# Optimization experiments

Hardware: AMD Instinct MI355X
Metric: run time of the kernel (lower is better)

## Reference

```python
import jax, jax.numpy as jnp
import numpy as np

N_NODES = 50000
N_EDGES = 800000
G_DIM = 128
H1_DIM = 128
H2_DIM = 128
N_REL = 8          # 2 * n_speakers**2, n_speakers = 2
N_BASES = 30


def setup_inputs() -> dict:
    key = jax.random.key(0)
    ks = jax.random.split(key, 10)
    node_features = jax.random.normal(ks[0], (N_NODES, G_DIM), jnp.float32)
    edge_index = jax.random.randint(ks[1], (2, N_EDGES), 0, N_NODES, jnp.int32)
    edge_norm = jax.random.uniform(ks[2], (N_EDGES,), jnp.float32)
    edge_type = jax.random.randint(ks[3], (N_EDGES,), 0, N_REL, jnp.int32)
    # RGCN basis-decomposition params
    w_comp = jax.random.normal(ks[4], (N_REL, N_BASES), jnp.float32) / np.sqrt(N_BASES)
    bases = jax.random.normal(ks[5], (N_BASES, G_DIM, H1_DIM), jnp.float32) / np.sqrt(G_DIM)
    loop_weight = jax.random.normal(ks[6], (G_DIM, H1_DIM), jnp.float32) / np.sqrt(G_DIM)
    bias1 = jnp.zeros((H1_DIM,), jnp.float32)
    # GraphConv params
    W2 = jax.random.normal(ks[7], (H1_DIM, H2_DIM), jnp.float32) / np.sqrt(H1_DIM)
    bias2 = jnp.zeros((H2_DIM,), jnp.float32)
    return dict(node_features=node_features, edge_index=edge_index,
                edge_norm=edge_norm, edge_type=edge_type,
                w_comp=w_comp, bases=bases, loop_weight=loop_weight, bias1=bias1,
                W2=W2, bias2=bias2)


def reference(node_features, edge_index, edge_norm, edge_type,
              w_comp, bases, loop_weight, bias1, W2, bias2):
    N = node_features.shape[0]
    src, dst = edge_index[0], edge_index[1]

    # ---- RGCNConv (DGL RelGraphConv, basis regularizer, self_loop + bias) ----
    # relation weights from bases: [R, g, h1]
    weight = jnp.einsum('rb,bio->rio', w_comp, bases)
    # project all nodes by every relation (R is small), then gather per edge
    xw = jnp.einsum('ni,rio->rno', node_features, weight)   # [R, N, h1]
    msgs = xw[edge_type, src] * edge_norm[:, None]          # [E, h1]
    agg = jax.ops.segment_sum(msgs, dst, num_segments=N)    # scatter-add to dst
    h = agg + node_features @ loop_weight + bias1           # [N, h1]

    # ---- GraphConv (DGL, norm='both', edge_weight; degrees are UNweighted) ----
    ones = jnp.ones_like(edge_norm)
    out_deg = jax.ops.segment_sum(ones, src, num_segments=N)
    in_deg = jax.ops.segment_sum(ones, dst, num_segments=N)
    norm_src = jnp.clip(out_deg, 1.0) ** -0.5               # [N]
    norm_dst = jnp.clip(in_deg, 1.0) ** -0.5                # [N]
    m2 = (h * norm_src[:, None])[src] * edge_norm[:, None]  # [E, h1]
    agg2 = jax.ops.segment_sum(m2, dst, num_segments=N)     # [N, h1]
    out = (agg2 * norm_dst[:, None]) @ W2 + bias2           # [N, h2]
    return out
```

## Files before the change

### kernel.cpp

```cpp
#include <hip/hip_runtime.h>

#define NN 50000
#define EE 800000
#define NB 30
#define NJ 1152
#define NSB 49
#define NPART 16
#define RANGE 3136
#define NSLICE 64
#define ESL 12500
#define NPAD 50176

typedef __attribute__((ext_vector_type(8))) short short8;
typedef __attribute__((ext_vector_type(4))) float f32x4;

__device__ __forceinline__ unsigned short f2bf(float f) {
  unsigned u = __float_as_uint(f);
  u += 0x7FFF + ((u >> 16) & 1);
  return (unsigned short)(u >> 16);
}
__device__ __forceinline__ float bf2f(unsigned short s) {
  return __uint_as_float(((unsigned)s) << 16);
}

__global__ __launch_bounds__(256) void k_prep(const float* __restrict__ wcomp,
                                              const float* __restrict__ bases,
                                              const float* __restrict__ loopw,
                                              const float* __restrict__ W2,
                                              const float* __restrict__ X,
                                              unsigned short* __restrict__ Wt,
                                              unsigned short* __restrict__ W2t,
                                              unsigned short* __restrict__ Xbf) {
  int b = blockIdx.x;
  if (b < 576) {
    int idx = b * 256 + threadIdx.x;
    int j = idx >> 7, k = idx & 127;
    float v;
    if (j < 1024) {
      int r = j >> 7, o = j & 127;
      float s = 0.f;
#pragma unroll
      for (int bb = 0; bb < NB; ++bb)
        s = fmaf(wcomp[r * NB + bb], bases[((size_t)bb * 128 + k) * 128 + o], s);
      v = s;
    } else {
      v = loopw[k * 128 + (j - 1024)];
    }
    Wt[idx] = f2bf(v);
    if (idx < 128 * 128) W2t[idx] = f2bf(W2[k * 128 + j]);
  } else {
    int i = ((b - 576) * 256 + threadIdx.x) * 4;
    float4 v = *(const float4*)(X + i);
    uint2 o;
    o.x = (unsigned)f2bf(v.x) | ((unsigned)f2bf(v.y) << 16);
    o.y = (unsigned)f2bf(v.z) | ((unsigned)f2bf(v.w) << 16);
    *(uint2*)(Xbf + i) = o;
  }
}

__global__ __launch_bounds__(256) void k_hist(const int* __restrict__ EI,
                                              int* __restrict__ pdin, int* __restrict__ pdout) {
  __shared__ int hist[RANGE];
  int b = blockIdx.x;
  int kind = b & 1;
  int sl = (b >> 1) & (NSLICE - 1);
  int r = b >> 7;
  const int base = r * RANGE;
  const int* vals = kind ? EI : EI + EE;
  int* part = kind ? pdout : pdin;
  for (int j = threadIdx.x; j < RANGE; j += 256) hist[j] = 0;
  __syncthreads();
  const int e0 = sl * ESL;
  for (int i = threadIdx.x; i < ESL / 4; i += 256) {
    int4 d = *(const int4*)(vals + e0 + i * 4);
    int x;
    x = d.x - base; if ((unsigned)x < RANGE) atomicAdd(&hist[x], 1);
    x = d.y - base; if ((unsigned)x < RANGE) atomicAdd(&hist[x], 1);
    x = d.z - base; if ((unsigned)x < RANGE) atomicAdd(&hist[x], 1);
    x = d.w - base; if ((unsigned)x < RANGE) atomicAdd(&hist[x], 1);
  }
  __syncthreads();
  for (int j = threadIdx.x; j < RANGE; j += 256)
    part[sl * NPAD + base + j] = hist[j];
}

__global__ __launch_bounds__(256) void k_scan_a(const int* __restrict__ pdin,
                                                const int* __restrict__ pdout,
                                                int* __restrict__ din,
                                                int* __restrict__ dout,
                                                int* __restrict__ bsum) {
  __shared__ int wsum[4];
  int b = blockIdx.x, t = threadIdx.x;
  int lane = t & 63, w = t >> 6;
  int i0 = b * 1024 + t * 4;
  int4 acc = {0, 0, 0, 0}, od = {0, 0, 0, 0};
  for (int sl = 0; sl < NSLICE; ++sl) {
    int4 a = *(const int4*)(pdin + sl * NPAD + i0);
    int4 o = *(const int4*)(pdout + sl * NPAD + i0);
    acc.x += a.x; acc.y += a.y; acc.z += a.z; acc.w += a.w;
    od.x += o.x; od.y += o.y; od.z += o.z; od.w += o.w;
  }
  *(int4*)(din + i0) = acc;
  *(int4*)(dout + i0) = od;
  int sv = acc.x + acc.y + acc.z + acc.w;
#pragma unroll
  for (int off = 32; off; off >>= 1) sv += __shfl_down(sv, off, 64);
  if (lane == 0) wsum[w] = sv;
  __syncthreads();
  if (t == 0) bsum[b] = wsum[0] + wsum[1] + wsum[2] + wsum[3];
}

__global__ void k_scan_b(int* __restrict__ bsum, int* __restrict__ row_ptr) {
  int t = threadIdx.x;
  int v = (t < NSB) ? bsum[t] : 0;
  int orig = v;
#pragma unroll
  for (int off = 1; off < 64; off <<= 1) {
    int u = __shfl_up(v, off, 64);
    if (t >= off) v += u;
  }
  if (t < NSB) bsum[t] = v - orig;
  if (t == 0) row_ptr[NN] = EE;
}

__global__ __launch_bounds__(256) void k_scan_c(const int* __restrict__ din,
                                                const int* __restrict__ bsum,
                                                int* __restrict__ row_ptr) {
  __shared__ int wsum[4];
  int b = blockIdx.x, t = threadIdx.x;
  int lane = t & 63, w = t >> 6;
  int i0 = b * 1024 + t * 4;
  int4 d = *(const int4*)(din + i0);
  int sth = d.x + d.y + d.z + d.w;
  int v = sth;
#pragma unroll
  for (int off = 1; off < 64; off <<= 1) {
    int u = __shfl_up(v, off, 64);
    if (lane >= off) v += u;
  }
  if (lane == 63) wsum[w] = v;
  __syncthreads();
  int woff = 0;
  for (int j = 0; j < w; ++j) woff += wsum[j];
  int base = bsum[b] + woff + (v - sth);
  if (i0 + 0 <= NN) row_ptr[i0 + 0] = base; base += d.x;
  if (i0 + 1 <= NN) row_ptr[i0 + 1] = base; base += d.y;
  if (i0 + 2 <= NN) row_ptr[i0 + 2] = base; base += d.z;
  if (i0 + 3 <= NN) row_ptr[i0 + 3] = base;
}

__global__ __launch_bounds__(256) void k_pfx(int* __restrict__ pdin,
                                             const int* __restrict__ row_ptr) {
  int n = blockIdx.x * 256 + threadIdx.x;
  int run = row_ptr[n];
#pragma unroll 8
  for (int sl = 0; sl < NSLICE; ++sl) {
    int c = pdin[sl * NPAD + n];
    pdin[sl * NPAD + n] = run;
    run += c;
  }
}

__global__ __launch_bounds__(256) void k_scatter(const int* __restrict__ src,
                                                 const int* __restrict__ dst,
                                                 const int* __restrict__ ety,
                                                 const float* __restrict__ enorm,
                                                 const int* __restrict__ pdin,
                                                 int2* __restrict__ em1) {
  __shared__ int cur[RANGE];
  int b = blockIdx.x;
  int sl = b & (NSLICE - 1), r = b >> 6;
  const int base = r * RANGE;
  for (int j = threadIdx.x; j < RANGE; j += 256)
    cur[j] = pdin[sl * NPAD + base + j];
  __syncthreads();
  const int e0 = sl * ESL;
  for (int i = threadIdx.x; i < ESL / 4; i += 256) {
    int4 d = *(const int4*)(dst + e0 + i * 4);
    int vals[4] = {d.x, d.y, d.z, d.w};
#pragma unroll
    for (int j = 0; j < 4; ++j) {
      int dv = vals[j] - base;
      if ((unsigned)dv < RANGE) {
        int e = e0 + i * 4 + j;
        int pos = atomicAdd(&cur[dv], 1);
        int sv = src[e];
        int wb = __float_as_int(enorm[e]);
        em1[pos] = make_int2(sv * NJ + ety[e] * 128, wb);
      }
    }
  }
}

__global__ __launch_bounds__(256) void k_gemm(const unsigned short* __restrict__ A,
                                              const unsigned short* __restrict__ B,
                                              unsigned short* __restrict__ Cbf,
                                              float* __restrict__ Cf,
                                              const float* __restrict__ bias,
                                              int M, int ldc) {
  __shared__ unsigned short As[128 * 136];
  __shared__ unsigned short Bs[128 * 136];
  const int m0 = blockIdx.x * 128, j0 = blockIdx.y * 128;
  const int t = threadIdx.x;
  for (int i = t; i < 2048; i += 256) {
    int r = i >> 4, c = i & 15;
    uint4 va = {0, 0, 0, 0};
    int gr = m0 + r;
    if (gr < M) va = *(const uint4*)(A + (size_t)gr * 128 + c * 8);
    *(uint4*)(&As[r * 136 + c * 8]) = va;
    uint4 vb = *(const uint4*)(B + (size_t)(j0 + r) * 128 + c * 8);
    *(uint4*)(&Bs[r * 136 + c * 8]) = vb;
  }
  __syncthreads();

  const int lane = t & 63, wave = t >> 6;
  const int wr = (wave >> 1) * 64, wc = (wave & 1) * 64;
  const int lr = lane & 15, lk = (lane >> 4) * 8;

  f32x4 acc[4][4];
#pragma unroll
  for (int m = 0; m < 4; ++m)
#pragma unroll
    for (int n = 0; n < 4; ++n) acc[m][n] = (f32x4){0.f, 0.f, 0.f, 0.f};

#pragma unroll
  for (int kt = 0; kt < 4; ++kt) {
    short8 af[4], bfr[4];
#pragma unroll
    for (int m = 0; m < 4; ++m)
      af[m] = *(const short8*)(&As[(wr + m * 16 + lr) * 136 + kt * 32 + lk]);
#pragma unroll
    for (int n = 0; n < 4; ++n)
      bfr[n] = *(const short8*)(&Bs[(wc + n * 16 + lr) * 136 + kt * 32 + lk]);
#pragma unroll
    for (int m = 0; m < 4; ++m)
#pragma unroll
      for (int n = 0; n < 4; ++n)
        acc[m][n] = __builtin_amdgcn_mfma_f32_16x16x32_bf16(af[m], bfr[n], acc[m][n], 0, 0, 0);
  }

#pragma unroll
  for (int m = 0; m < 4; ++m) {
    int rbase = m0 + wr + m * 16 + (lane >> 4) * 4;
#pragma unroll
    for (int i = 0; i < 4; ++i) {
      int row = rbase + i;
      if (row >= M) continue;
      if (Cbf) {
        unsigned short* cr = Cbf + (size_t)row * ldc + j0 + wc;
#pragma unroll
        for (int n = 0; n < 4; ++n) cr[n * 16 + lr] = f2bf(acc[m][n][i]);
      } else {
        float* cr = Cf + (size_t)row * ldc + j0 + wc;
#pragma unroll
        for (int n = 0; n < 4; ++n) cr[n * 16 + lr] = acc[m][n][i] + bias[j0 + wc + n * 16 + lr];
      }
    }
  }
}

#define UNR 8

__global__ __launch_bounds__(256) void k_agg1(const unsigned short* __restrict__ xw,
                                              const int2* __restrict__ em1,
                                              const int* __restrict__ row_ptr,
                                              const int* __restrict__ deg_out,
                                              const float* __restrict__ bias1,
                                              unsigned short* __restrict__ hs) {
  int gw = (blockIdx.x * blockDim.x + threadIdx.x) >> 6;
  int lane = threadIdx.x & 63;
  if (gw >= NN) return;
  int beg = row_ptr[gw], end = row_ptr[gw + 1];
  float a0 = 0.f, a1 = 0.f;
  for (int i = beg; i < end; i += UNR) {
    int2 md[UNR];
    unsigned v[UNR];
#pragma unroll
    for (int j = 0; j < UNR; ++j) {
      int idx = i + j;
      idx = idx < end ? idx : end - 1;
      md[j] = em1[idx];
      if (i + j >= end) md[j].y = 0;
    }
#pragma unroll
    for (int j = 0; j < UNR; ++j)
      v[j] = *(const unsigned*)(xw + (size_t)(unsigned)md[j].x + lane * 2);
#pragma unroll
    for (int j = 0; j < UNR; ++j) {
      float w = __int_as_float(md[j].y);
      a0 = fmaf(w, bf2f((unsigned short)(v[j] & 0xffff)), a0);
      a1 = fmaf(w, bf2f((unsigned short)(v[j] >> 16)), a1);
    }
  }
  unsigned vl = *(const unsigned*)(xw + (size_t)gw * NJ + 1024 + lane * 2);
  float ns = rsqrtf(fmaxf((float)deg_out[gw], 1.f));
  float h0 = (a0 + bf2f((unsigned short)(vl & 0xffff)) + bias1[lane * 2]) * ns;
  float h1 = (a1 + bf2f((unsigned short)(vl >> 16)) + bias1[lane * 2 + 1]) * ns;
  unsigned o = (unsigned)f2bf(h0) | ((unsigned)f2bf(h1) << 16);
  *(unsigned*)(hs + (size_t)gw * 128 + lane * 2) = o;
}

__global__ __launch_bounds__(256) void k_agg2(const unsigned short* __restrict__ hs,
                                              const int2* __restrict__ em1,
                                              const int* __restrict__ row_ptr,
                                              unsigned short* __restrict__ zb) {
  int gw = (blockIdx.x * blockDim.x + threadIdx.x) >> 6;
  int lane = threadIdx.x & 63;
  if (gw >= NN) return;
  int beg = row_ptr[gw], end = row_ptr[gw + 1];
  float a0 = 0.f, a1 = 0.f;
  for (int i = beg; i < end; i += UNR) {
    int2 md[UNR];
    unsigned v[UNR];
#pragma unroll
    for (int j = 0; j < UNR; ++j) {
      int idx = i + j;
      idx = idx < end ? idx : end - 1;
      md[j] = em1[idx];
      if (i + j >= end) md[j].y = 0;
    }
#pragma unroll
    for (int j = 0; j < UNR; ++j) {
      unsigned srcn = (((unsigned)md[j].x) >> 7) / 9u;
      v[j] = *(const unsigned*)(hs + ((size_t)srcn << 7) + lane * 2);
    }
#pragma unroll
    for (int j = 0; j < UNR; ++j) {
      float w = __int_as_float(md[j].y);
      a0 = fmaf(w, bf2f((unsigned short)(v[j] & 0xffff)), a0);
      a1 = fmaf(w, bf2f((unsigned short)(v[j] >> 16)), a1);
    }
  }
  float nd = rsqrtf(fmaxf((float)(end - beg), 1.f));
  unsigned o = (unsigned)f2bf(a0 * nd) | ((unsigned)f2bf(a1 * nd) << 16);
  *(unsigned*)(zb + (size_t)gw * 128 + lane * 2) = o;
}

extern "C" void kernel_launch(void* const* d_in, const int* in_sizes, int n_in,
                              void* d_out, int out_size, void* d_ws, size_t ws_size,
                              hipStream_t stream) {
  const float* X = (const float*)d_in[0];
  const int* EI = (const int*)d_in[1];
  const float* enorm = (const float*)d_in[2];
  const int* etype = (const int*)d_in[3];
  const float* wcomp = (const float*)d_in[4];
  const float* bases = (const float*)d_in[5];
  const float* loopw = (const float*)d_in[6];
  const float* bias1 = (const float*)d_in[7];
  const float* W2 = (const float*)d_in[8];
  const float* bias2 = (const float*)d_in[9];
  float* out = (float*)d_out;
  const int* srcA = EI;
  const int* dstA = EI + EE;

  char* p = (char*)d_ws;
  auto alloc = [&](size_t bytes) {
    char* r = p;
    p += (bytes + 255) & ~(size_t)255;
    return r;
  };
  unsigned short* xw  = (unsigned short*)alloc((size_t)NN * NJ * 2);
  unsigned short* Xbf = (unsigned short*)alloc((size_t)NN * 128 * 2);
  unsigned short* hs  = (unsigned short*)alloc((size_t)NN * 128 * 2);
  unsigned short* zb  = (unsigned short*)alloc((size_t)NN * 128 * 2);
  unsigned short* Wt  = (unsigned short*)alloc((size_t)NJ * 128 * 2);
  unsigned short* W2t = (unsigned short*)alloc(128 * 128 * 2);
  int* pdin    = (int*)alloc((size_t)NSLICE * NPAD * 4);
  int* pdout   = (int*)alloc((size_t)NSLICE * NPAD * 4);
  int* din     = (int*)alloc((size_t)NPAD * 4);
  int* dout    = (int*)alloc((size_t)NPAD * 4);
  int* row_ptr = (int*)alloc((size_t)(NPAD + 1) * 4);
  int* bsum    = (int*)alloc((size_t)NSB * 4);
  int2* em1    = (int2*)alloc((size_t)EE * 8);

  hipLaunchKernelGGL(k_prep, dim3(6826), dim3(256), 0, stream,
                     wcomp, bases, loopw, W2, X, Wt, W2t, Xbf);
  hipLaunchKernelGGL(k_hist, dim3(2048), dim3(256), 0, stream, EI, pdin, pdout);
  hipLaunchKernelGGL(k_scan_a, dim3(NSB), dim3(256), 0, stream, pdin, pdout, din, dout, bsum);
  hipLaunchKernelGGL(k_scan_b, dim3(1), dim3(64), 0, stream, bsum, row_ptr);
  hipLaunchKernelGGL(k_scan_c, dim3(NSB), dim3(256), 0, stream, din, bsum, row_ptr);
  hipLaunchKernelGGL(k_pfx, dim3(NPAD / 256), dim3(256), 0, stream, pdin, row_ptr);
  hipLaunchKernelGGL(k_scatter, dim3(1024), dim3(256), 0, stream,
                     srcA, dstA, etype, enorm, pdin, em1);
  hipLaunchKernelGGL(k_gemm, dim3(391, 9), dim3(256), 0, stream,
                     Xbf, Wt, xw, (float*)nullptr, (const float*)nullptr, NN, NJ);
  hipLaunchKernelGGL(k_agg1, dim3(12500), dim3(256), 0, stream,
                     xw, em1, row_ptr, dout, bias1, hs);
  hipLaunchKernelGGL(k_agg2, dim3(12500), dim3(256), 0, stream,
                     hs, em1, row_ptr, zb);
  hipLaunchKernelGGL(k_gemm, dim3(391, 1), dim3(256), 0, stream,
                     zb, W2t, (unsigned short*)nullptr, out, bias2, NN, 128);
}
```

Before: 325.3 us.

## Aggregate raw features per relation first, then apply stacked relation weights via GEMM

Reorders layer-1 RGCN as aggregate-then-transform. Each destination node gathers bf16 input features (256 B rows) and accumulates per-relation sums into a [N,8*128] buffer. A single K=1152 GEMM then applies the stacked relation and self-loop weights, fusing bias and source-degree normalization into its epilogue. This replaces the gather of 128-wide rows from the large 50000x1152 projected table, which has a poor cache footprint, with gathers from a much smaller table. The cost is more FMAs per edge (8 masked relation accumulators), a 100 MB intermediate write and read, and an extra K loop in the GEMM.

```diff
diff --git a/kernel.cpp b/kernel.cpp
--- a/kernel.cpp
+++ b/kernel.cpp
@@ -3,7 +3,7 @@
 #define NN 50000
 #define EE 800000
 #define NB 30
-#define NJ 1152
+#define NK2 1152
 #define NSB 49
 #define NPART 16
 #define RANGE 3136
@@ -28,26 +28,30 @@
                                               const float* __restrict__ loopw,
                                               const float* __restrict__ W2,
                                               const float* __restrict__ X,
-                                              unsigned short* __restrict__ Wt,
+                                              unsigned short* __restrict__ Wt2,
                                               unsigned short* __restrict__ W2t,
                                               unsigned short* __restrict__ Xbf) {
   int b = blockIdx.x;
   if (b < 576) {
     int idx = b * 256 + threadIdx.x;
-    int j = idx >> 7, k = idx & 127;
+    int o = idx & 127;
+    int ri = idx >> 7;
+    int r = ri >> 7, i = ri & 127;
     float v;
-    if (j < 1024) {
-      int r = j >> 7, o = j & 127;
+    if (r < 8) {
       float s = 0.f;
 #pragma unroll
       for (int bb = 0; bb < NB; ++bb)
-        s = fmaf(wcomp[r * NB + bb], bases[((size_t)bb * 128 + k) * 128 + o], s);
+        s = fmaf(wcomp[r * NB + bb], bases[((size_t)bb * 128 + i) * 128 + o], s);
       v = s;
     } else {
-      v = loopw[k * 128 + (j - 1024)];
-    }
-    Wt[idx] = f2bf(v);
-    if (idx < 128 * 128) W2t[idx] = f2bf(W2[k * 128 + j]);
+      v = loopw[i * 128 + o];
+    }
+    Wt2[(size_t)o * NK2 + ri] = f2bf(v);
+    if (idx < 128 * 128) {
+      int j = idx >> 7, k = idx & 127;
+      W2t[idx] = f2bf(W2[k * 128 + j]);
+    }
   } else {
     int i = ((b - 576) * 256 + threadIdx.x) * 4;
     float4 v = *(const float4*)(X + i);
@@ -166,7 +170,7 @@
                                                  const int* __restrict__ ety,
                                                  const float* __restrict__ enorm,
                                                  const int* __restrict__ pdin,
-                                                 int2* __restrict__ em1) {
+                                                 int2* __restrict__ em) {
   __shared__ int cur[RANGE];
   int b = blockIdx.x;
   int sl = b & (NSLICE - 1), r = b >> 6;
@@ -184,94 +188,25 @@
       if ((unsigned)dv < RANGE) {
         int e = e0 + i * 4 + j;
         int pos = atomicAdd(&cur[dv], 1);
-        int sv = src[e];
-        int wb = __float_as_int(enorm[e]);
-        em1[pos] = make_int2(sv * NJ + ety[e] * 128, wb);
+        em[pos] = make_int2((src[e] << 4) | ety[e], __float_as_int(enorm[e]));
       }
     }
   }
 }
 
-__global__ __launch_bounds__(256) void k_gemm(const unsigned short* __restrict__ A,
-                                              const unsigned short* __restrict__ B,
-                                              unsigned short* __restrict__ Cbf,
-                                              float* __restrict__ Cf,
-                                              const float* __restrict__ bias,
-                                              int M, int ldc) {
-  __shared__ unsigned short As[128 * 136];
-  __shared__ unsigned short Bs[128 * 136];
-  const int m0 = blockIdx.x * 128, j0 = blockIdx.y * 128;
-  const int t = threadIdx.x;
-  for (int i = t; i < 2048; i += 256) {
-    int r = i >> 4, c = i & 15;
-    uint4 va = {0, 0, 0, 0};
-    int gr = m0 + r;
-    if (gr < M) va = *(const uint4*)(A + (size_t)gr * 128 + c * 8);
-    *(uint4*)(&As[r * 136 + c * 8]) = va;
-    uint4 vb = *(const uint4*)(B + (size_t)(j0 + r) * 128 + c * 8);
-    *(uint4*)(&Bs[r * 136 + c * 8]) = vb;
-  }
-  __syncthreads();
-
-  const int lane = t & 63, wave = t >> 6;
-  const int wr = (wave >> 1) * 64, wc = (wave & 1) * 64;
-  const int lr = lane & 15, lk = (lane >> 4) * 8;
-
-  f32x4 acc[4][4];
-#pragma unroll
-  for (int m = 0; m < 4; ++m)
-#pragma unroll
-    for (int n = 0; n < 4; ++n) acc[m][n] = (f32x4){0.f, 0.f, 0.f, 0.f};
-
-#pragma unroll
-  for (int kt = 0; kt < 4; ++kt) {
-    short8 af[4], bfr[4];
-#pragma unroll
-    for (int m = 0; m < 4; ++m)
-      af[m] = *(const short8*)(&As[(wr + m * 16 + lr) * 136 + kt * 32 + lk]);
-#pragma unroll
-    for (int n = 0; n < 4; ++n)
-      bfr[n] = *(const short8*)(&Bs[(wc + n * 16 + lr) * 136 + kt * 32 + lk]);
-#pragma unroll
-    for (int m = 0; m < 4; ++m)
-#pragma unroll
-      for (int n = 0; n < 4; ++n)
-        acc[m][n] = __builtin_amdgcn_mfma_f32_16x16x32_bf16(af[m], bfr[n], acc[m][n], 0, 0, 0);
-  }
-
-#pragma unroll
-  for (int m = 0; m < 4; ++m) {
-    int rbase = m0 + wr + m * 16 + (lane >> 4) * 4;
-#pragma unroll
-    for (int i = 0; i < 4; ++i) {
-      int row = rbase + i;
-      if (row >= M) continue;
-      if (Cbf) {
-        unsigned short* cr = Cbf + (size_t)row * ldc + j0 + wc;
-#pragma unroll
-        for (int n = 0; n < 4; ++n) cr[n * 16 + lr] = f2bf(acc[m][n][i]);
-      } else {
-        float* cr = Cf + (size_t)row * ldc + j0 + wc;
-#pragma unroll
-        for (int n = 0; n < 4; ++n) cr[n * 16 + lr] = acc[m][n][i] + bias[j0 + wc + n * 16 + lr];
-      }
-    }
-  }
-}
-
 #define UNR 8
 
-__global__ __launch_bounds__(256) void k_agg1(const unsigned short* __restrict__ xw,
-                                              const int2* __restrict__ em1,
+__global__ __launch_bounds__(256) void k_agg0(const unsigned short* __restrict__ Xbf,
+                                              const int2* __restrict__ em,
                                               const int* __restrict__ row_ptr,
-                                              const int* __restrict__ deg_out,
-                                              const float* __restrict__ bias1,
-                                              unsigned short* __restrict__ hs) {
+                                              unsigned short* __restrict__ Y) {
   int gw = (blockIdx.x * blockDim.x + threadIdx.x) >> 6;
   int lane = threadIdx.x & 63;
   if (gw >= NN) return;
   int beg = row_ptr[gw], end = row_ptr[gw + 1];
-  float a0 = 0.f, a1 = 0.f;
+  float a0[8], a1[8];
+#pragma unroll
+  for (int r = 0; r < 8; ++r) { a0[r] = 0.f; a1[r] = 0.f; }
   for (int i = beg; i < end; i += UNR) {
     int2 md[UNR];
     unsigned v[UNR];
@@ -279,29 +214,107 @@
     for (int j = 0; j < UNR; ++j) {
       int idx = i + j;
       idx = idx < end ? idx : end - 1;
-      md[j] = em1[idx];
+      md[j] = em[idx];
       if (i + j >= end) md[j].y = 0;
     }
 #pragma unroll
     for (int j = 0; j < UNR; ++j)
-      v[j] = *(const unsigned*)(xw + (size_t)(unsigned)md[j].x + lane * 2);
+      v[j] = *(const unsigned*)(Xbf + ((size_t)((unsigned)md[j].x >> 4) << 7) + lane * 2);
 #pragma unroll
     for (int j = 0; j < UNR; ++j) {
       float w = __int_as_float(md[j].y);
-      a0 = fmaf(w, bf2f((unsigned short)(v[j] & 0xffff)), a0);
-      a1 = fmaf(w, bf2f((unsigned short)(v[j] >> 16)), a1);
-    }
-  }
-  unsigned vl = *(const unsigned*)(xw + (size_t)gw * NJ + 1024 + lane * 2);
-  float ns = rsqrtf(fmaxf((float)deg_out[gw], 1.f));
-  float h0 = (a0 + bf2f((unsigned short)(vl & 0xffff)) + bias1[lane * 2]) * ns;
-  float h1 = (a1 + bf2f((unsigned short)(vl >> 16)) + bias1[lane * 2 + 1]) * ns;
-  unsigned o = (unsigned)f2bf(h0) | ((unsigned)f2bf(h1) << 16);
-  *(unsigned*)(hs + (size_t)gw * 128 + lane * 2) = o;
+      int ty = md[j].x & 15;
+      float x0 = bf2f((unsigned short)(v[j] & 0xffff));
+      float x1 = bf2f((unsigned short)(v[j] >> 16));
+#pragma unroll
+      for (int r = 0; r < 8; ++r) {
+        float ws = (ty == r) ? w : 0.f;
+        a0[r] = fmaf(ws, x0, a0[r]);
+        a1[r] = fmaf(ws, x1, a1[r]);
+      }
+    }
+  }
+  unsigned short* yr = Y + (size_t)gw * 1024 + lane * 2;
+#pragma unroll
+  for (int r = 0; r < 8; ++r) {
+    unsigned o = (unsigned)f2bf(a0[r]) | ((unsigned)f2bf(a1[r]) << 16);
+    *(unsigned*)(yr + r * 128) = o;
+  }
+}
+
+__global__ __launch_bounds__(256) void k_gemmh(const unsigned short* __restrict__ Y,
+                                               const unsigned short* __restrict__ Xbf,
+                                               const unsigned short* __restrict__ Wt2,
+                                               const int* __restrict__ dout,
+                                               const float* __restrict__ bias1,
+                                               unsigned short* __restrict__ hs) {
+  __shared__ unsigned short As[64 * 136];
+  __shared__ unsigned short Bs[128 * 136];
+  const int m0 = blockIdx.x * 64;
+  const int t = threadIdx.x;
+  const int lane = t & 63, wave = t >> 6;
+  const int wr = (wave >> 1) * 32, wc = (wave & 1) * 64;
+  const int lr = lane & 15, lk = (lane >> 4) * 8;
+
+  f32x4 acc[2][4];
+#pragma unroll
+  for (int m = 0; m < 2; ++m)
+#pragma unroll
+    for (int n = 0; n < 4; ++n) acc[m][n] = (f32x4){0.f, 0.f, 0.f, 0.f};
+
+  for (int kt = 0; kt < 9; ++kt) {
+    __syncthreads();
+    for (int i = t; i < 1024; i += 256) {
+      int r = i >> 4, c = i & 15;
+      int n = m0 + r;
+      uint4 va = {0, 0, 0, 0};
+      if (n < NN) {
+        const unsigned short* ap = (kt < 8) ? (Y + (size_t)n * 1024 + kt * 128)
+                                            : (Xbf + (size_t)n * 128);
+        va = *(const uint4*)(ap + c * 8);
+      }
+      *(uint4*)(&As[r * 136 + c * 8]) = va;
+    }
+    for (int i = t; i < 2048; i += 256) {
+      int r = i >> 4, c = i & 15;
+      uint4 vb = *(const uint4*)(Wt2 + (size_t)r * NK2 + kt * 128 + c * 8);
+      *(uint4*)(&Bs[r * 136 + c * 8]) = vb;
+    }
+    __syncthreads();
+#pragma unroll
+    for (int s = 0; s < 4; ++s) {
+      short8 af[2], bfv[4];
+#pragma unroll
+      for (int m = 0; m < 2; ++m)
+        af[m] = *(const short8*)(&As[(wr + m * 16 + lr) * 136 + s * 32 + lk]);
+#pragma unroll
+      for (int n = 0; n < 4; ++n)
+        bfv[n] = *(const short8*)(&Bs[(wc + n * 16 + lr) * 136 + s * 32 + lk]);
+#pragma unroll
+      for (int m = 0; m < 2; ++m)
+#pragma unroll
+        for (int n = 0; n < 4; ++n)
+          acc[m][n] = __builtin_amdgcn_mfma_f32_16x16x32_bf16(af[m], bfv[n], acc[m][n], 0, 0, 0);
+    }
+  }
+
+#pragma unroll
+  for (int m = 0; m < 2; ++m) {
+#pragma unroll
+    for (int i = 0; i < 4; ++i) {
+      int row = m0 + wr + m * 16 + (lane >> 4) * 4 + i;
+      if (row >= NN) continue;
+      float ns = rsqrtf(fmaxf((float)dout[row], 1.f));
+      unsigned short* hr = hs + (size_t)row * 128 + wc;
+#pragma unroll
+      for (int n = 0; n < 4; ++n)
+        hr[n * 16 + lr] = f2bf((acc[m][n][i] + bias1[wc + n * 16 + lr]) * ns);
+    }
+  }
 }
 
 __global__ __launch_bounds__(256) void k_agg2(const unsigned short* __restrict__ hs,
-                                              const int2* __restrict__ em1,
+                                              const int2* __restrict__ em,
                                               const int* __restrict__ row_ptr,
                                               unsigned short* __restrict__ zb) {
   int gw = (blockIdx.x * blockDim.x + threadIdx.x) >> 6;
@@ -316,14 +329,12 @@
     for (int j = 0; j < UNR; ++j) {
       int idx = i + j;
       idx = idx < end ? idx : end - 1;
-      md[j] = em1[idx];
+      md[j] = em[idx];
       if (i + j >= end) md[j].y = 0;
     }
 #pragma unroll
-    for (int j = 0; j < UNR; ++j) {
-      unsigned srcn = (((unsigned)md[j].x) >> 7) / 9u;
-      v[j] = *(const unsigned*)(hs + ((size_t)srcn << 7) + lane * 2);
-    }
+    for (int j = 0; j < UNR; ++j)
+      v[j] = *(const unsigned*)(hs + ((size_t)((unsigned)md[j].x >> 4) << 7) + lane * 2);
 #pragma unroll
     for (int j = 0; j < UNR; ++j) {
       float w = __int_as_float(md[j].y);
@@ -334,6 +345,66 @@
   float nd = rsqrtf(fmaxf((float)(end - beg), 1.f));
   unsigned o = (unsigned)f2bf(a0 * nd) | ((unsigned)f2bf(a1 * nd) << 16);
   *(unsigned*)(zb + (size_t)gw * 128 + lane * 2) = o;
+}
+
+__global__ __launch_bounds__(256) void k_gemm(const unsigned short* __restrict__ A,
+                                              const unsigned short* __restrict__ B,
+                                              float* __restrict__ Cf,
+                                              const float* __restrict__ bias,
+                                              int M, int ldc) {
+  __shared__ unsigned short As[128 * 136];
+  __shared__ unsigned short Bs[128 * 136];
+  const int m0 = blockIdx.x * 128, j0 = 0;
+  const int t = threadIdx.x;
+  for (int i = t; i < 2048; i += 256) {
+    int r = i >> 4, c = i & 15;
+    uint4 va = {0, 0, 0, 0};
+    int gr = m0 + r;
+    if (gr < M) va = *(const uint4*)(A + (size_t)gr * 128 + c * 8);
+    *(uint4*)(&As[r * 136 + c * 8]) = va;
+    uint4 vb = *(const uint4*)(B + (size_t)(j0 + r) * 128 + c * 8);
+    *(uint4*)(&Bs[r * 136 + c * 8]) = vb;
+  }
+  __syncthreads();
+
+  const int lane = t & 63, wave = t >> 6;
+  const int wr = (wave >> 1) * 64, wc = (wave & 1) * 64;
+  const int lr = lane & 15, lk = (lane >> 4) * 8;
+
+  f32x4 acc[4][4];
+#pragma unroll
+  for (int m = 0; m < 4; ++m)
+#pragma unroll
+    for (int n = 0; n < 4; ++n) acc[m][n] = (f32x4){0.f, 0.f, 0.f, 0.f};
+
+#pragma unroll
+  for (int kt = 0; kt < 4; ++kt) {
+    short8 af[4], bfr[4];
+#pragma unroll
+    for (int m = 0; m < 4; ++m)
+      af[m] = *(const short8*)(&As[(wr + m * 16 + lr) * 136 + kt * 32 + lk]);
+#pragma unroll
+    for (int n = 0; n < 4; ++n)
+      bfr[n] = *(const short8*)(&Bs[(wc + n * 16 + lr) * 136 + kt * 32 + lk]);
+#pragma unroll
+    for (int m = 0; m < 4; ++m)
+#pragma unroll
+      for (int n = 0; n < 4; ++n)
+        acc[m][n] = __builtin_amdgcn_mfma_f32_16x16x32_bf16(af[m], bfr[n], acc[m][n], 0, 0, 0);
+  }
+
+#pragma unroll
+  for (int m = 0; m < 4; ++m) {
+    int rbase = m0 + wr + m * 16 + (lane >> 4) * 4;
+#pragma unroll
+    for (int i = 0; i < 4; ++i) {
+      int row = rbase + i;
+      if (row >= M) continue;
+      float* cr = Cf + (size_t)row * ldc + j0 + wc;
+#pragma unroll
+      for (int n = 0; n < 4; ++n) cr[n * 16 + lr] = acc[m][n][i] + bias[j0 + wc + n * 16 + lr];
+    }
+  }
 }
 
 extern "C" void kernel_launch(void* const* d_in, const int* in_sizes, int n_in,
@@ -359,11 +430,11 @@
     p += (bytes + 255) & ~(size_t)255;
     return r;
   };
-  unsigned short* xw  = (unsigned short*)alloc((size_t)NN * NJ * 2);
+  unsigned short* Y   = (unsigned short*)alloc((size_t)NN * 1024 * 2);
   unsigned short* Xbf = (unsigned short*)alloc((size_t)NN * 128 * 2);
   unsigned short* hs  = (unsigned short*)alloc((size_t)NN * 128 * 2);
   unsigned short* zb  = (unsigned short*)alloc((size_t)NN * 128 * 2);
-  unsigned short* Wt  = (unsigned short*)alloc((size_t)NJ * 128 * 2);
+  unsigned short* Wt2 = (unsigned short*)alloc((size_t)128 * NK2 * 2);
   unsigned short* W2t = (unsigned short*)alloc(128 * 128 * 2);
   int* pdin    = (int*)alloc((size_t)NSLICE * NPAD * 4);
   int* pdout   = (int*)alloc((size_t)NSLICE * NPAD * 4);
@@ -371,23 +442,21 @@
   int* dout    = (int*)alloc((size_t)NPAD * 4);
   int* row_ptr = (int*)alloc((size_t)(NPAD + 1) * 4);
   int* bsum    = (int*)alloc((size_t)NSB * 4);
-  int2* em1    = (int2*)alloc((size_t)EE * 8);
+  int2* em     = (int2*)alloc((size_t)EE * 8);
 
   hipLaunchKernelGGL(k_prep, dim3(6826), dim3(256), 0, stream,
-                     wcomp, bases, loopw, W2, X, Wt, W2t, Xbf);
+                     wcomp, bases, loopw, W2, X, Wt2, W2t, Xbf);
   hipLaunchKernelGGL(k_hist, dim3(2048), dim3(256), 0, stream, EI, pdin, pdout);
   hipLaunchKernelGGL(k_scan_a, dim3(NSB), dim3(256), 0, stream, pdin, pdout, din, dout, bsum);
   hipLaunchKernelGGL(k_scan_b, dim3(1), dim3(64), 0, stream, bsum, row_ptr);
   hipLaunchKernelGGL(k_scan_c, dim3(NSB), dim3(256), 0, stream, din, bsum, row_ptr);
   hipLaunchKernelGGL(k_pfx, dim3(NPAD / 256), dim3(256), 0, stream, pdin, row_ptr);
   hipLaunchKernelGGL(k_scatter, dim3(1024), dim3(256), 0, stream,
-                     srcA, dstA, etype, enorm, pdin, em1);
-  hipLaunchKernelGGL(k_gemm, dim3(391, 9), dim3(256), 0, stream,
-                     Xbf, Wt, xw, (float*)nullptr, (const float*)nullptr, NN, NJ);
-  hipLaunchKernelGGL(k_agg1, dim3(12500), dim3(256), 0, stream,
-                     xw, em1, row_ptr, dout, bias1, hs);
-  hipLaunchKernelGGL(k_agg2, dim3(12500), dim3(256), 0, stream,
-                     hs, em1, row_ptr, zb);
-  hipLaunchKernelGGL(k_gemm, dim3(391, 1), dim3(256), 0, stream,
-                     zb, W2t, (unsigned short*)nullptr, out, bias2, NN, 128);
-}
+                     srcA, dstA, etype, enorm, pdin, em);
+  hipLaunchKernelGGL(k_agg0, dim3(12500), dim3(256), 0, stream, Xbf, em, row_ptr, Y);
+  hipLaunchKernelGGL(k_gemmh, dim3(782), dim3(256), 0, stream,
+                     Y, Xbf, Wt2, dout, bias1, hs);
+  hipLaunchKernelGGL(k_agg2, dim3(12500), dim3(256), 0, stream, hs, em, row_ptr, zb);
+  hipLaunchKernelGGL(k_gemm, dim3(391), dim3(256), 0, stream,
+                     zb, W2t, out, bias2, NN, 128);
+}
```

Result: slower. 355.5 us (+9.3%).

## Fuse prep with histogram, drop scan_b launch, specialize GEMMs with direct B loads

Applied to the files above, without the earlier changes.

Merges the weight/feature bf16 conversion kernel with the degree histogram kernel into one launch, and removes the single-block block-sum scan by having each scan_c block sum preceding block totals itself. The first GEMM is specialized: it no longer stages B in shared memory, reading B fragments directly from global (L2-resident weights), halves LDS use and sets launch bounds for 4 blocks per CU to raise occupancy. The second GEMM becomes its own specialized kernel. The aim is fewer launches and better occupancy, at the cost of uncoalesced global B reads in gemm1.

```diff
diff --git a/kernel.cpp b/kernel.cpp
--- a/kernel.cpp
+++ b/kernel.cpp
@@ -23,14 +23,18 @@
   return __uint_as_float(((unsigned)s) << 16);
 }
 
-__global__ __launch_bounds__(256) void k_prep(const float* __restrict__ wcomp,
-                                              const float* __restrict__ bases,
-                                              const float* __restrict__ loopw,
-                                              const float* __restrict__ W2,
-                                              const float* __restrict__ X,
-                                              unsigned short* __restrict__ Wt,
-                                              unsigned short* __restrict__ W2t,
-                                              unsigned short* __restrict__ Xbf) {
+__global__ __launch_bounds__(256) void k_prep_hist(const float* __restrict__ wcomp,
+                                                   const float* __restrict__ bases,
+                                                   const float* __restrict__ loopw,
+                                                   const float* __restrict__ W2,
+                                                   const float* __restrict__ X,
+                                                   const int* __restrict__ EI,
+                                                   unsigned short* __restrict__ Wt,
+                                                   unsigned short* __restrict__ W2t,
+                                                   unsigned short* __restrict__ Xbf,
+                                                   int* __restrict__ pdin,
+                                                   int* __restrict__ pdout) {
+  __shared__ int hist[RANGE];
   int b = blockIdx.x;
   if (b < 576) {
     int idx = b * 256 + threadIdx.x;
@@ -48,40 +52,36 @@
     }
     Wt[idx] = f2bf(v);
     if (idx < 128 * 128) W2t[idx] = f2bf(W2[k * 128 + j]);
-  } else {
+  } else if (b < 6826) {
     int i = ((b - 576) * 256 + threadIdx.x) * 4;
     float4 v = *(const float4*)(X + i);
     uint2 o;
     o.x = (unsigned)f2bf(v.x) | ((unsigned)f2bf(v.y) << 16);
     o.y = (unsigned)f2bf(v.z) | ((unsigned)f2bf(v.w) << 16);
     *(uint2*)(Xbf + i) = o;
-  }
-}
-
-__global__ __launch_bounds__(256) void k_hist(const int* __restrict__ EI,
-                                              int* __restrict__ pdin, int* __restrict__ pdout) {
-  __shared__ int hist[RANGE];
-  int b = blockIdx.x;
-  int kind = b & 1;
-  int sl = (b >> 1) & (NSLICE - 1);
-  int r = b >> 7;
-  const int base = r * RANGE;
-  const int* vals = kind ? EI : EI + EE;
-  int* part = kind ? pdout : pdin;
-  for (int j = threadIdx.x; j < RANGE; j += 256) hist[j] = 0;
-  __syncthreads();
-  const int e0 = sl * ESL;
-  for (int i = threadIdx.x; i < ESL / 4; i += 256) {
-    int4 d = *(const int4*)(vals + e0 + i * 4);
-    int x;
-    x = d.x - base; if ((unsigned)x < RANGE) atomicAdd(&hist[x], 1);
-    x = d.y - base; if ((unsigned)x < RANGE) atomicAdd(&hist[x], 1);
-    x = d.z - base; if ((unsigned)x < RANGE) atomicAdd(&hist[x], 1);
-    x = d.w - base; if ((unsigned)x < RANGE) atomicAdd(&hist[x], 1);
-  }
-  __syncthreads();
-  for (int j = threadIdx.x; j < RANGE; j += 256)
-    part[sl * NPAD + base + j] = hist[j];
+  } else {
+    int b2 = b - 6826;
+    int kind = b2 & 1;
+    int sl = (b2 >> 1) & (NSLICE - 1);
+    int r = b2 >> 7;
+    const int base = r * RANGE;
+    const int* vals = kind ? EI : EI + EE;
+    int* part = kind ? pdout : pdin;
+    for (int j = threadIdx.x; j < RANGE; j += 256) hist[j] = 0;
+    __syncthreads();
+    const int e0 = sl * ESL;
+    for (int i = threadIdx.x; i < ESL / 4; i += 256) {
+      int4 d = *(const int4*)(vals + e0 + i * 4);
+      int x;
+      x = d.x - base; if ((unsigned)x < RANGE) atomicAdd(&hist[x], 1);
+      x = d.y - base; if ((unsigned)x < RANGE) atomicAdd(&hist[x], 1);
+      x = d.z - base; if ((unsigned)x < RANGE) atomicAdd(&hist[x], 1);
+      x = d.w - base; if ((unsigned)x < RANGE) atomicAdd(&hist[x], 1);
+    }
+    __syncthreads();
+    for (int j = threadIdx.x; j < RANGE; j += 256)
+      part[sl * NPAD + base + j] = hist[j];
+  }
 }
 
 __global__ __launch_bounds__(256) void k_scan_a(const int* __restrict__ pdin,
@@ -110,19 +110,6 @@
   if (t == 0) bsum[b] = wsum[0] + wsum[1] + wsum[2] + wsum[3];
 }
 
-__global__ void k_scan_b(int* __restrict__ bsum, int* __restrict__ row_ptr) {
-  int t = threadIdx.x;
-  int v = (t < NSB) ? bsum[t] : 0;
-  int orig = v;
-#pragma unroll
-  for (int off = 1; off < 64; off <<= 1) {
-    int u = __shfl_up(v, off, 64);
-    if (t >= off) v += u;
-  }
-  if (t < NSB) bsum[t] = v - orig;
-  if (t == 0) row_ptr[NN] = EE;
-}
-
 __global__ __launch_bounds__(256) void k_scan_c(const int* __restrict__ din,
                                                 const int* __restrict__ bsum,
                                                 int* __restrict__ row_ptr) {
@@ -142,7 +129,9 @@
   __syncthreads();
   int woff = 0;
   for (int j = 0; j < w; ++j) woff += wsum[j];
-  int base = bsum[b] + woff + (v - sth);
+  int boff = 0;
+  for (int j = 0; j < b; ++j) boff += bsum[j];
+  int base = boff + woff + (v - sth);
   if (i0 + 0 <= NN) row_ptr[i0 + 0] = base; base += d.x;
   if (i0 + 1 <= NN) row_ptr[i0 + 1] = base; base += d.y;
   if (i0 + 2 <= NN) row_ptr[i0 + 2] = base; base += d.z;
@@ -166,7 +155,7 @@
                                                  const int* __restrict__ ety,
                                                  const float* __restrict__ enorm,
                                                  const int* __restrict__ pdin,
-                                                 int2* __restrict__ em1) {
+                                                 int2* __restrict__ em) {
   __shared__ int cur[RANGE];
   int b = blockIdx.x;
   int sl = b & (NSLICE - 1), r = b >> 6;
@@ -184,32 +173,24 @@
       if ((unsigned)dv < RANGE) {
         int e = e0 + i * 4 + j;
         int pos = atomicAdd(&cur[dv], 1);
-        int sv = src[e];
-        int wb = __float_as_int(enorm[e]);
-        em1[pos] = make_int2(sv * NJ + ety[e] * 128, wb);
+        em[pos] = make_int2(src[e] * NJ + ety[e] * 128, __float_as_int(enorm[e]));
       }
     }
   }
 }
 
-__global__ __launch_bounds__(256) void k_gemm(const unsigned short* __restrict__ A,
-                                              const unsigned short* __restrict__ B,
-                                              unsigned short* __restrict__ Cbf,
-                                              float* __restrict__ Cf,
-                                              const float* __restrict__ bias,
-                                              int M, int ldc) {
+__global__ __launch_bounds__(256, 4) void k_gemm1(const unsigned short* __restrict__ A,
+                                                  const unsigned short* __restrict__ B,
+                                                  unsigned short* __restrict__ C) {
   __shared__ unsigned short As[128 * 136];
-  __shared__ unsigned short Bs[128 * 136];
   const int m0 = blockIdx.x * 128, j0 = blockIdx.y * 128;
   const int t = threadIdx.x;
   for (int i = t; i < 2048; i += 256) {
     int r = i >> 4, c = i & 15;
     uint4 va = {0, 0, 0, 0};
     int gr = m0 + r;
-    if (gr < M) va = *(const uint4*)(A + (size_t)gr * 128 + c * 8);
+    if (gr < NN) va = *(const uint4*)(A + (size_t)gr * 128 + c * 8);
     *(uint4*)(&As[r * 136 + c * 8]) = va;
-    uint4 vb = *(const uint4*)(B + (size_t)(j0 + r) * 128 + c * 8);
-    *(uint4*)(&Bs[r * 136 + c * 8]) = vb;
   }
   __syncthreads();
 
@@ -225,18 +206,18 @@
 
 #pragma unroll
   for (int kt = 0; kt < 4; ++kt) {
-    short8 af[4], bfr[4];
+    short8 af[4], bfv[4];
+#pragma unroll
+    for (int n = 0; n < 4; ++n)
+      bfv[n] = *(const short8*)(B + (size_t)(j0 + wc + n * 16 + lr) * 128 + kt * 32 + lk);
 #pragma unroll
     for (int m = 0; m < 4; ++m)
       af[m] = *(const short8*)(&As[(wr + m * 16 + lr) * 136 + kt * 32 + lk]);
 #pragma unroll
-    for (int n = 0; n < 4; ++n)
-      bfr[n] = *(const short8*)(&Bs[(wc + n * 16 + lr) * 136 + kt * 32 + lk]);
-#pragma unroll
     for (int m = 0; m < 4; ++m)
 #pragma unroll
       for (int n = 0; n < 4; ++n)
-        acc[m][n] = __builtin_amdgcn_mfma_f32_16x16x32_bf16(af[m], bfr[n], acc[m][n], 0, 0, 0);
+        acc[m][n] = __builtin_amdgcn_mfma_f32_16x16x32_bf16(af[m], bfv[n], acc[m][n], 0, 0, 0);
   }
 
 #pragma unroll
@@ -245,16 +226,10 @@
 #pragma unroll
     for (int i = 0; i < 4; ++i) {
       int row = rbase + i;
-      if (row >= M) continue;
-      if (Cbf) {
-        unsigned short* cr = Cbf + (size_t)row * ldc + j0 + wc;
-#pragma unroll
-        for (int n = 0; n < 4; ++n) cr[n * 16 + lr] = f2bf(acc[m][n][i]);
-      } else {
-        float* cr = Cf + (size_t)row * ldc + j0 + wc;
-#pragma unroll
-        for (int n = 0; n < 4; ++n) cr[n * 16 + lr] = acc[m][n][i] + bias[j0 + wc + n * 16 + lr];
-      }
+      if (row >= NN) continue;
+      unsigned short* cr = C + (size_t)row * NJ + j0 + wc;
+#pragma unroll
+      for (int n = 0; n < 4; ++n) cr[n * 16 + lr] = f2bf(acc[m][n][i]);
     }
   }
 }
@@ -262,7 +237,7 @@
 #define UNR 8
 
 __global__ __launch_bounds__(256) void k_agg1(const unsigned short* __restrict__ xw,
-                                              const int2* __restrict__ em1,
+                                              const int2* __restrict__ em,
                                               const int* __restrict__ row_ptr,
                                               const int* __restrict__ deg_out,
                                               const float* __restrict__ bias1,
@@ -279,7 +254,7 @@
     for (int j = 0; j < UNR; ++j) {
       int idx = i + j;
       idx = idx < end ? idx : end - 1;
-      md[j] = em1[idx];
+      md[j] = em[idx];
       if (i + j >= end) md[j].y = 0;
     }
 #pragma unroll
@@ -301,7 +276,7 @@
 }
 
 __global__ __launch_bounds__(256) void k_agg2(const unsigned short* __restrict__ hs,
-                                              const int2* __restrict__ em1,
+                                              const int2* __restrict__ em,
                                               const int* __restrict__ row_ptr,
                                               unsigned short* __restrict__ zb) {
   int gw = (blockIdx.x * blockDim.x + threadIdx.x) >> 6;
@@ -316,7 +291,7 @@
     for (int j = 0; j < UNR; ++j) {
       int idx = i + j;
       idx = idx < end ? idx : end - 1;
-      md[j] = em1[idx];
+      md[j] = em[idx];
       if (i + j >= end) md[j].y = 0;
     }
 #pragma unroll
@@ -334,6 +309,65 @@
   float nd = rsqrtf(fmaxf((float)(end - beg), 1.f));
   unsigned o = (unsigned)f2bf(a0 * nd) | ((unsigned)f2bf(a1 * nd) << 16);
   *(unsigned*)(zb + (size_t)gw * 128 + lane * 2) = o;
+}
+
+__global__ __launch_bounds__(256) void k_gemm2(const unsigned short* __restrict__ A,
+                                               const unsigned short* __restrict__ B,
+                                               float* __restrict__ Cf,
+                                               const float* __restrict__ bias) {
+  __shared__ unsigned short As[128 * 136];
+  __shared__ unsigned short Bs[128 * 136];
+  const int m0 = blockIdx.x * 128;
+  const int t = threadIdx.x;
+  for (int i = t; i < 2048; i += 256) {
+    int r = i >> 4, c = i & 15;
+    uint4 va = {0, 0, 0, 0};
+    int gr = m0 + r;
+    if (gr < NN) va = *(const uint4*)(A + (size_t)gr * 128 + c * 8);
+    *(uint4*)(&As[r * 136 + c * 8]) = va;
+    uint4 vb = *(const uint4*)(B + (size_t)r * 128 + c * 8);
+    *(uint4*)(&Bs[r * 136 + c * 8]) = vb;
+  }
+  __syncthreads();
+
+  const int lane = t & 63, wave = t >> 6;
+  const int wr = (wave >> 1) * 64, wc = (wave & 1) * 64;
+  const int lr = lane & 15, lk = (lane >> 4) * 8;
+
+  f32x4 acc[4][4];
+#pragma unroll
+  for (int m = 0; m < 4; ++m)
+#pragma unroll
+    for (int n = 0; n < 4; ++n) acc[m][n] = (f32x4){0.f, 0.f, 0.f, 0.f};
+
+#pragma unroll
+  for (int kt = 0; kt < 4; ++kt) {
+    short8 af[4], bfr[4];
+#pragma unroll
+    for (int m = 0; m < 4; ++m)
+      af[m] = *(const short8*)(&As[(wr + m * 16 + lr) * 136 + kt * 32 + lk]);
+#pragma unroll
+    for (int n = 0; n < 4; ++n)
+      bfr[n] = *(const short8*)(&Bs[(wc + n * 16 + lr) * 136 + kt * 32 + lk]);
+#pragma unroll
+    for (int m = 0; m < 4; ++m)
+#pragma unroll
+      for (int n = 0; n < 4; ++n)
+        acc[m][n] = __builtin_amdgcn_mfma_f32_16x16x32_bf16(af[m], bfr[n], acc[m][n], 0, 0, 0);
+  }
+
+#pragma unroll
+  for (int m = 0; m < 4; ++m) {
+    int rbase = m0 + wr + m * 16 + (lane >> 4) * 4;
+#pragma unroll
+    for (int i = 0; i < 4; ++i) {
+      int row = rbase + i;
+      if (row >= NN) continue;
+      float* cr = Cf + (size_t)row * 128 + wc;
+#pragma unroll
+      for (int n = 0; n < 4; ++n) cr[n * 16 + lr] = acc[m][n][i] + bias[wc + n * 16 + lr];
+    }
+  }
 }
 
 extern "C" void kernel_launch(void* const* d_in, const int* in_sizes, int n_in,
@@ -371,23 +405,18 @@
   int* dout    = (int*)alloc((size_t)NPAD * 4);
   int* row_ptr = (int*)alloc((size_t)(NPAD + 1) * 4);
   int* bsum    = (int*)alloc((size_t)NSB * 4);
-  int2* em1    = (int2*)alloc((size_t)EE * 8);
-
-  hipLaunchKernelGGL(k_prep, dim3(6826), dim3(256), 0, stream,
-                     wcomp, bases, loopw, W2, X, Wt, W2t, Xbf);
-  hipLaunchKernelGGL(k_hist, dim3(2048), dim3(256), 0, stream, EI, pdin, pdout);
+  int2* em     = (int2*)alloc((size_t)EE * 8);
+
+  hipLaunchKernelGGL(k_prep_hist, dim3(8874), dim3(256), 0, stream,
+                     wcomp, bases, loopw, W2, X, EI, Wt, W2t, Xbf, pdin, pdout);
   hipLaunchKernelGGL(k_scan_a, dim3(NSB), dim3(256), 0, stream, pdin, pdout, din, dout, bsum);
-  hipLaunchKernelGGL(k_scan_b, dim3(1), dim3(64), 0, stream, bsum, row_ptr);
   hipLaunchKernelGGL(k_scan_c, dim3(NSB), dim3(256), 0, stream, din, bsum, row_ptr);
   hipLaunchKernelGGL(k_pfx, dim3(NPAD / 256), dim3(256), 0, stream, pdin, row_ptr);
   hipLaunchKernelGGL(k_scatter, dim3(1024), dim3(256), 0, stream,
-                     srcA, dstA, etype, enorm, pdin, em1);
-  hipLaunchKernelGGL(k_gemm, dim3(391, 9), dim3(256), 0, stream,
-                     Xbf, Wt, xw, (float*)nullptr, (const float*)nullptr, NN, NJ);
+                     srcA, dstA, etype, enorm, pdin, em);
+  hipLaunchKernelGGL(k_gemm1, dim3(391, 9), dim3(256), 0, stream, Xbf, Wt, xw);
   hipLaunchKernelGGL(k_agg1, dim3(12500), dim3(256), 0, stream,
-                     xw, em1, row_ptr, dout, bias1, hs);
-  hipLaunchKernelGGL(k_agg2, dim3(12500), dim3(256), 0, stream,
-                     hs, em1, row_ptr, zb);
-  hipLaunchKernelGGL(k_gemm, dim3(391, 1), dim3(256), 0, stream,
-                     zb, W2t, (unsigned short*)nullptr, out, bias2, NN, 128);
-}
+                     xw, em, row_ptr, dout, bias1, hs);
+  hipLaunchKernelGGL(k_agg2, dim3(12500), dim3(256), 0, stream, hs, em, row_ptr, zb);
+  hipLaunchKernelGGL(k_gemm2, dim3(391), dim3(256), 0, stream, zb, W2t, out, bias2);
+}
```

After: 339.7 us. +4.4%, slower.
